# Kernel optimization log

Hardware: AMD Instinct MI355X
Metric: run time of the kernel (lower is better)

The kernel has to match this reference:

```python
import jax, jax.numpy as jnp
import numpy as np

BATCH = 2048
IN_DIM = 512          # group input dim
HID = 1024            # meta_output_dim = dim*2
E = 16                # meta_experts_num = num_experts*2
RANK = 2              # lora_rank
EPS = 1e-5


def setup_inputs() -> dict:
    key = jax.random.key(0)
    ks = jax.random.split(key, 8)
    x = jax.random.normal(ks[0], (BATCH, IN_DIM), jnp.float32)
    gate_states = jax.random.normal(ks[1], (BATCH, IN_DIM), jnp.float32)
    expert_indices = jnp.arange(E, dtype=jnp.int64)
    expert_weights = jax.random.normal(ks[2], (E, IN_DIM, HID), jnp.float32) * 0.02
    expert_biases = jnp.zeros((E, HID), jnp.float32)
    bn_weights = jnp.ones((E, HID), jnp.float32)
    bn_biases = jnp.zeros((E, HID), jnp.float32)
    running_mean = jax.random.normal(ks[3], (E, HID), jnp.float32) * 0.1
    running_var = jnp.abs(jax.random.normal(ks[4], (E, HID), jnp.float32)) * 0.5 + 0.5
    gate_weights = jax.random.normal(ks[5], (IN_DIM, E), jnp.float32) * 0.02
    lora_A = jax.random.normal(ks[6], (IN_DIM, RANK), jnp.float32) * 0.02
    lora_B = jax.random.normal(ks[7], (RANK, IN_DIM), jnp.float32) * 0.02
    return dict(x=x, gate_states=gate_states, expert_indices=expert_indices,
                expert_weights=expert_weights, expert_biases=expert_biases,
                bn_weights=bn_weights, bn_biases=bn_biases,
                running_mean=running_mean, running_var=running_var,
                gate_weights=gate_weights, lora_A=lora_A, lora_B=lora_B)


def reference(x, gate_states, expert_indices, expert_weights, expert_biases,
              bn_weights, bn_biases, running_mean, running_var,
              gate_weights, lora_A, lora_B):
    # LoRA feature gate (lora_gate_forward with sigmoid): x * sigmoid(x A B)
    xg = x * jax.nn.sigmoid((x @ lora_A) @ lora_B)          # [B, D]

    # Expert dispatch: gather selected expert params (home_expert_forward)
    W = expert_weights[expert_indices]                        # [E, D, H]
    b = expert_biases[expert_indices]                         # [E, H]
    h = jnp.einsum('bd,edh->ebh', xg, W) + b[:, None, :]      # [E, B, H]

    # Fused inference BatchNorm + SiLU (fused_batch_norm_silu_forward)
    inv = jax.lax.rsqrt(running_var[expert_indices] + EPS)    # [E, H]
    scale = bn_weights[expert_indices] * inv                  # [E, H]
    shift = bn_biases[expert_indices] - running_mean[expert_indices] * scale
    h = h * scale[:, None, :] + shift[:, None, :]
    h = h * jax.nn.sigmoid(h)                                 # SiLU

    # Softmax gate (gate_weights_forward) and weighted combine
    g = jax.nn.softmax(gate_states @ gate_weights, axis=-1)   # [B, E]
    out = jnp.einsum('ebh,be->bh', h, g)                      # [B, H]
    return out
```

## Files before the change

### kernel.cpp

```cpp
#include <hip/hip_runtime.h>
#include <hip/hip_bf16.h>

#define BATCH 2048
#define IN_DIM 512
#define HID 1024
#define NE 16
#define EPSV 1e-5f

typedef __bf16 bf16x8 __attribute__((ext_vector_type(8)));
typedef float floatx4 __attribute__((ext_vector_type(4)));
typedef unsigned short ushort8 __attribute__((ext_vector_type(8)));

__device__ __forceinline__ unsigned short f2bf(float f) {
  unsigned int u = __builtin_bit_cast(unsigned int, f);
  u += 0x7FFFu + ((u >> 16) & 1u);
  return (unsigned short)(u >> 16);
}

__device__ __forceinline__ int get_expert(const int* __restrict__ idx, int e) {
  bool is64 = (idx[1] == 0) && (idx[3] == 0);
  return is64 ? (int)((const long long*)idx)[e] : idx[e];
}

__device__ __forceinline__ void gld16(void* lds, const void* g) {
  __builtin_amdgcn_global_load_lds(
      (const __attribute__((address_space(1))) void*)g,
      (__attribute__((address_space(3))) void*)lds, 16, 0, 0);
}

__global__ __launch_bounds__(256) void zero_out(float* __restrict__ out) {
  int t = blockIdx.x * 256 + threadIdx.x;
  ((float4*)out)[t] = float4{0.f, 0.f, 0.f, 0.f};
}

__global__ __launch_bounds__(256) void prep_coef(
    const int* __restrict__ idx, const float* __restrict__ bnw,
    const float* __restrict__ bnb, const float* __restrict__ rmean,
    const float* __restrict__ rvar, const float* __restrict__ ebias,
    float* __restrict__ Ac, float* __restrict__ Cc) {
  int t = blockIdx.x * 256 + threadIdx.x;
  int e = t >> 10, h = t & 1023;
  int ie = get_expert(idx, e);
  size_t o = (size_t)ie * HID + h;
  float scale = bnw[o] * rsqrtf(rvar[o] + EPSV);
  Ac[t] = scale;
  Cc[t] = (ebias[o] - rmean[o]) * scale + bnb[o];
}

__global__ __launch_bounds__(256) void prep_rows(
    const float* __restrict__ x, const float* __restrict__ gs,
    const float* __restrict__ gw, const float* __restrict__ lA,
    const float* __restrict__ lB,
    unsigned short* __restrict__ xg, float* __restrict__ g) {
  int lane = threadIdx.x & 63;
  int wid = threadIdx.x >> 6;
  int b = blockIdx.x * 4 + wid;
  const float* xrow = x + (size_t)b * IN_DIM;
  const float* grow = gs + (size_t)b * IN_DIM;
  int d0 = lane * 8;

  float4 xa = *(const float4*)(xrow + d0);
  float4 xb = *(const float4*)(xrow + d0 + 4);
  float xv[8] = {xa.x, xa.y, xa.z, xa.w, xb.x, xb.y, xb.z, xb.w};
  float4 ga = *(const float4*)(grow + d0);
  float4 gb = *(const float4*)(grow + d0 + 4);
  float gv[8] = {ga.x, ga.y, ga.z, ga.w, gb.x, gb.y, gb.z, gb.w};

  float u0 = 0.f, u1 = 0.f;
#pragma unroll
  for (int j = 0; j < 8; ++j) {
    float2 a2 = *(const float2*)(lA + (size_t)(d0 + j) * 2);
    u0 += xv[j] * a2.x;
    u1 += xv[j] * a2.y;
  }
#pragma unroll
  for (int off = 1; off < 64; off <<= 1) {
    u0 += __shfl_xor(u0, off);
    u1 += __shfl_xor(u1, off);
  }

  float ge[16];
#pragma unroll
  for (int e = 0; e < 16; ++e) ge[e] = 0.f;
#pragma unroll
  for (int j = 0; j < 8; ++j) {
    float q = gv[j];
    const float4* gwr = (const float4*)(gw + (size_t)(d0 + j) * NE);
    float4 w0 = gwr[0], w1 = gwr[1], w2 = gwr[2], w3 = gwr[3];
    ge[0] += q * w0.x; ge[1] += q * w0.y; ge[2] += q * w0.z; ge[3] += q * w0.w;
    ge[4] += q * w1.x; ge[5] += q * w1.y; ge[6] += q * w1.z; ge[7] += q * w1.w;
    ge[8] += q * w2.x; ge[9] += q * w2.y; ge[10] += q * w2.z; ge[11] += q * w2.w;
    ge[12] += q * w3.x; ge[13] += q * w3.y; ge[14] += q * w3.z; ge[15] += q * w3.w;
  }
#pragma unroll
  for (int off = 1; off < 64; off <<= 1) {
#pragma unroll
    for (int e = 0; e < 16; ++e) ge[e] += __shfl_xor(ge[e], off);
  }
  float m = ge[0];
#pragma unroll
  for (int e = 1; e < 16; ++e) m = fmaxf(m, ge[e]);
  float p[16], s = 0.f;
#pragma unroll
  for (int e = 0; e < 16; ++e) { p[e] = __expf(ge[e] - m); s += p[e]; }
  float inv = 1.f / s;
  if (lane == 0) {
    float* gout = g + (size_t)b * NE;
#pragma unroll
    for (int e = 0; e < 16; ++e) gout[e] = p[e] * inv;
  }

  ushort8 ov;
#pragma unroll
  for (int j = 0; j < 8; ++j) {
    float t = u0 * lB[d0 + j] + u1 * lB[IN_DIM + d0 + j];
    float sg = 1.f / (1.f + __expf(-t));
    ov[j] = f2bf(xv[j] * sg);
  }
  *(ushort8*)(xg + (size_t)b * IN_DIM + d0) = ov;
}

__global__ __launch_bounds__(256) void prep_tw(
    const int* __restrict__ idx, const float* __restrict__ W,
    unsigned short* __restrict__ WT) {
  int bid = blockIdx.x;
  int e = bid >> 7;
  int kt = (bid >> 4) & 7;
  int ht = bid & 15;
  int ie = get_expert(idx, e);
  int k0 = kt * 64, h0 = ht * 64;
  __shared__ float tile[64][65];
  const float* Wp = W + (size_t)ie * IN_DIM * HID;
#pragma unroll
  for (int i = 0; i < 4; ++i) {
    int id = threadIdx.x + i * 256;
    int k = id >> 4, c = (id & 15) * 4;
    float4 v = *(const float4*)(Wp + (size_t)(k0 + k) * HID + h0 + c);
    tile[k][c] = v.x; tile[k][c + 1] = v.y; tile[k][c + 2] = v.z; tile[k][c + 3] = v.w;
  }
  __syncthreads();
#pragma unroll
  for (int i = 0; i < 2; ++i) {
    int id = threadIdx.x + i * 256;
    int h = id >> 3, kc = (id & 7) * 8;
    ushort8 o;
#pragma unroll
    for (int j = 0; j < 8; ++j) o[j] = f2bf(tile[kc + j][h]);
    *(ushort8*)(WT + ((size_t)e * HID + h0 + h) * IN_DIM + k0 + kc) = o;
  }
}

#define BM 128
#define BN 128
#define BK 32
#define EPB 4

__global__ __launch_bounds__(256, 2) void moe_main(
    const unsigned short* __restrict__ xg, const unsigned short* __restrict__ WT,
    const float* __restrict__ g, const float* __restrict__ Ac,
    const float* __restrict__ Cc, float* __restrict__ out) {
  __shared__ __align__(16) unsigned short As[2][BM * BK];
  __shared__ __align__(16) unsigned short Bs[2][BN * BK];
  __shared__ float gS[BM][EPB];

  int tid = threadIdx.x;
  int lane = tid & 63, w = tid >> 6;
  int wr = w >> 1, wc = w & 1;
  int l15 = lane & 15, quad = lane >> 4;

  int bid = blockIdx.x;
  int p = bid >> 7;
  int rowb = (bid >> 3) & 15, colb = bid & 7;
  int row0 = rowb * BM, col0 = colb * BN;
  int e0 = p * EPB;

  for (int i = tid; i < BM * EPB; i += 256) {
    int r = i >> 2, e = i & 3;
    gS[r][e] = g[(size_t)(row0 + r) * NE + e0 + e];
  }

  int dr = lane >> 2, dk = (lane & 3) * 8;
  const unsigned short* gA = xg + (size_t)(row0 + w * 32 + dr) * IN_DIM + dk;
  const unsigned short* gB0 = WT + ((size_t)e0 * HID + col0 + w * 32 + dr) * IN_DIM + dk;

  auto dma = [&](int t, int buf) {
    int e = t >> 4, k0 = (t & 15) * BK;
    const unsigned short* a = gA + k0;
    const unsigned short* b = gB0 + (size_t)e * HID * IN_DIM + k0;
#pragma unroll
    for (int j = 0; j < 2; ++j) {
      gld16(&As[buf][(w * 32 + j * 16) * BK], a + (size_t)j * 16 * IN_DIM);
      gld16(&Bs[buf][(w * 32 + j * 16) * BK], b + (size_t)j * 16 * IN_DIM);
    }
  };

  floatx4 acc[4][4], oacc[4][4];
#pragma unroll
  for (int rt = 0; rt < 4; ++rt)
#pragma unroll
    for (int ct = 0; ct < 4; ++ct)
#pragma unroll
      for (int r = 0; r < 4; ++r) { acc[rt][ct][r] = 0.f; oacc[rt][ct][r] = 0.f; }

  dma(0, 0);
  __syncthreads();
  int buf = 0;
  for (int t = 0; t < EPB * 16; ++t) {
    if (t < EPB * 16 - 1) dma(t + 1, buf ^ 1);
    bf16x8 af[4], bf[4];
#pragma unroll
    for (int rt = 0; rt < 4; ++rt)
      af[rt] = *(const bf16x8*)&As[buf][(wr * 64 + rt * 16 + l15) * BK + quad * 8];
#pragma unroll
    for (int ct = 0; ct < 4; ++ct)
      bf[ct] = *(const bf16x8*)&Bs[buf][(wc * 64 + ct * 16 + l15) * BK + quad * 8];
#pragma unroll
    for (int rt = 0; rt < 4; ++rt)
#pragma unroll
      for (int ct = 0; ct < 4; ++ct)
        acc[rt][ct] = __builtin_amdgcn_mfma_f32_16x16x32_bf16(af[rt], bf[ct], acc[rt][ct], 0, 0, 0);
    if ((t & 15) == 15) {
      int e = t >> 4;
#pragma unroll
      for (int ct = 0; ct < 4; ++ct) {
        int colg = col0 + wc * 64 + ct * 16 + l15;
        float A_ = Ac[(e0 + e) * HID + colg];
        float C_ = Cc[(e0 + e) * HID + colg];
#pragma unroll
        for (int rt = 0; rt < 4; ++rt) {
          int rb = wr * 64 + rt * 16 + quad * 4;
#pragma unroll
          for (int r = 0; r < 4; ++r) {
            float gvw = gS[rb + r][e];
            float z = A_ * acc[rt][ct][r] + C_;
            float sg = 1.f / (1.f + __expf(-z));
            oacc[rt][ct][r] += gvw * z * sg;
            acc[rt][ct][r] = 0.f;
          }
        }
      }
    }
    __syncthreads();
    buf ^= 1;
  }

#pragma unroll
  for (int rt = 0; rt < 4; ++rt)
#pragma unroll
    for (int ct = 0; ct < 4; ++ct)
#pragma unroll
      for (int r = 0; r < 4; ++r)
        atomicAdd(&out[(size_t)(row0 + wr * 64 + rt * 16 + quad * 4 + r) * HID +
                       col0 + wc * 64 + ct * 16 + l15], oacc[rt][ct][r]);
}

extern "C" void kernel_launch(void* const* d_in, const int* in_sizes, int n_in,
                              void* d_out, int out_size, void* d_ws, size_t ws_size,
                              hipStream_t stream) {
  const float* x     = (const float*)d_in[0];
  const float* gs    = (const float*)d_in[1];
  const int*   idx   = (const int*)d_in[2];
  const float* W     = (const float*)d_in[3];
  const float* ebias = (const float*)d_in[4];
  const float* bnw   = (const float*)d_in[5];
  const float* bnb   = (const float*)d_in[6];
  const float* rmean = (const float*)d_in[7];
  const float* rvar  = (const float*)d_in[8];
  const float* gw    = (const float*)d_in[9];
  const float* lA    = (const float*)d_in[10];
  const float* lB    = (const float*)d_in[11];
  float* out = (float*)d_out;

  char* ws = (char*)d_ws;
  unsigned short* WT = (unsigned short*)ws;
  unsigned short* xg = (unsigned short*)(ws + 16777216);
  float* g   = (float*)(ws + 18874368);
  float* Acf = (float*)(ws + 19005440);
  float* Ccf = (float*)(ws + 19070976);

  zero_out<<<dim3(BATCH * HID / 1024), dim3(256), 0, stream>>>(out);
  prep_coef<<<dim3(64), dim3(256), 0, stream>>>(idx, bnw, bnb, rmean, rvar, ebias, Acf, Ccf);
  prep_rows<<<dim3(BATCH / 4), dim3(256), 0, stream>>>(x, gs, gw, lA, lB, xg, g);
  prep_tw<<<dim3(2048), dim3(256), 0, stream>>>(idx, W, WT);
  moe_main<<<dim3((BATCH / BM) * (HID / BN) * (NE / EPB)), dim3(256), 0, stream>>>(
      xg, WT, g, Acf, Ccf, out);
}
```

Baseline: 197.3 us.

## Merge prep kernels, deepen K stage, replace atomics with split-buffer reduction

Combines the three prep kernels into one launch that dispatches on block index. The main GEMM loop now stages two 32-wide K slices per double-buffered step, which halves the number of barriers. When the workspace is large enough, each expert group writes its partial output to a separate buffer with plain stores, and a reduce kernel then sums the four buffers. This replaces the zero-fill plus atomicAdd path but costs extra memory traffic: 32MB written and read back, plus a larger LDS footprint.

```diff
diff --git a/kernel.cpp b/kernel.cpp
--- a/kernel.cpp
+++ b/kernel.cpp
@@ -28,139 +28,144 @@
       (__attribute__((address_space(3))) void*)lds, 16, 0, 0);
 }
 
+__global__ __launch_bounds__(256) void prep_all(
+    const int* __restrict__ idx, const float* __restrict__ W,
+    unsigned short* __restrict__ WT,
+    const float* __restrict__ x, const float* __restrict__ gs,
+    const float* __restrict__ gw, const float* __restrict__ lA,
+    const float* __restrict__ lB,
+    unsigned short* __restrict__ xg, float* __restrict__ g,
+    const float* __restrict__ bnw, const float* __restrict__ bnb,
+    const float* __restrict__ rmean, const float* __restrict__ rvar,
+    const float* __restrict__ ebias,
+    float* __restrict__ Ac, float* __restrict__ Cc) {
+  int bid = blockIdx.x;
+  if (bid < 2048) {
+    int e = bid >> 7, kt = (bid >> 4) & 7, ht = bid & 15;
+    int ie = get_expert(idx, e);
+    int k0 = kt * 64, h0 = ht * 64;
+    __shared__ float tile[64][65];
+    const float* Wp = W + (size_t)ie * IN_DIM * HID;
+#pragma unroll
+    for (int i = 0; i < 4; ++i) {
+      int id = threadIdx.x + i * 256;
+      int k = id >> 4, c = (id & 15) * 4;
+      float4 v = *(const float4*)(Wp + (size_t)(k0 + k) * HID + h0 + c);
+      tile[k][c] = v.x; tile[k][c + 1] = v.y; tile[k][c + 2] = v.z; tile[k][c + 3] = v.w;
+    }
+    __syncthreads();
+#pragma unroll
+    for (int i = 0; i < 2; ++i) {
+      int id = threadIdx.x + i * 256;
+      int h = id >> 3, kc = (id & 7) * 8;
+      ushort8 o;
+#pragma unroll
+      for (int j = 0; j < 8; ++j) o[j] = f2bf(tile[kc + j][h]);
+      *(ushort8*)(WT + ((size_t)e * HID + h0 + h) * IN_DIM + k0 + kc) = o;
+    }
+  } else if (bid < 2560) {
+    int lane = threadIdx.x & 63;
+    int b = (bid - 2048) * 4 + (threadIdx.x >> 6);
+    const float* xrow = x + (size_t)b * IN_DIM;
+    const float* grow = gs + (size_t)b * IN_DIM;
+    int d0 = lane * 8;
+    float4 xa = *(const float4*)(xrow + d0);
+    float4 xb = *(const float4*)(xrow + d0 + 4);
+    float xv[8] = {xa.x, xa.y, xa.z, xa.w, xb.x, xb.y, xb.z, xb.w};
+    float4 ga = *(const float4*)(grow + d0);
+    float4 gb = *(const float4*)(grow + d0 + 4);
+    float gv[8] = {ga.x, ga.y, ga.z, ga.w, gb.x, gb.y, gb.z, gb.w};
+
+    float u0 = 0.f, u1 = 0.f;
+#pragma unroll
+    for (int j = 0; j < 8; ++j) {
+      float2 a2 = *(const float2*)(lA + (size_t)(d0 + j) * 2);
+      u0 += xv[j] * a2.x;
+      u1 += xv[j] * a2.y;
+    }
+#pragma unroll
+    for (int off = 1; off < 64; off <<= 1) {
+      u0 += __shfl_xor(u0, off);
+      u1 += __shfl_xor(u1, off);
+    }
+    float ge[16];
+#pragma unroll
+    for (int e = 0; e < 16; ++e) ge[e] = 0.f;
+#pragma unroll
+    for (int j = 0; j < 8; ++j) {
+      float q = gv[j];
+      const float4* gwr = (const float4*)(gw + (size_t)(d0 + j) * NE);
+      float4 w0 = gwr[0], w1 = gwr[1], w2 = gwr[2], w3 = gwr[3];
+      ge[0] += q * w0.x; ge[1] += q * w0.y; ge[2] += q * w0.z; ge[3] += q * w0.w;
+      ge[4] += q * w1.x; ge[5] += q * w1.y; ge[6] += q * w1.z; ge[7] += q * w1.w;
+      ge[8] += q * w2.x; ge[9] += q * w2.y; ge[10] += q * w2.z; ge[11] += q * w2.w;
+      ge[12] += q * w3.x; ge[13] += q * w3.y; ge[14] += q * w3.z; ge[15] += q * w3.w;
+    }
+#pragma unroll
+    for (int off = 1; off < 64; off <<= 1) {
+#pragma unroll
+      for (int e = 0; e < 16; ++e) ge[e] += __shfl_xor(ge[e], off);
+    }
+    float m = ge[0];
+#pragma unroll
+    for (int e = 1; e < 16; ++e) m = fmaxf(m, ge[e]);
+    float p[16], s = 0.f;
+#pragma unroll
+    for (int e = 0; e < 16; ++e) { p[e] = __expf(ge[e] - m); s += p[e]; }
+    float inv = 1.f / s;
+    if (lane == 0) {
+      float* gout = g + (size_t)b * NE;
+#pragma unroll
+      for (int e = 0; e < 16; ++e) gout[e] = p[e] * inv;
+    }
+    ushort8 ov;
+#pragma unroll
+    for (int j = 0; j < 8; ++j) {
+      float t = u0 * lB[d0 + j] + u1 * lB[IN_DIM + d0 + j];
+      float sg = 1.f / (1.f + __expf(-t));
+      ov[j] = f2bf(xv[j] * sg);
+    }
+    *(ushort8*)(xg + (size_t)b * IN_DIM + d0) = ov;
+  } else {
+    int t = (bid - 2560) * 256 + threadIdx.x;
+    int e = t >> 10, h = t & 1023;
+    int ie = get_expert(idx, e);
+    size_t o = (size_t)ie * HID + h;
+    float scale = bnw[o] * rsqrtf(rvar[o] + EPSV);
+    Ac[t] = scale;
+    Cc[t] = (ebias[o] - rmean[o]) * scale + bnb[o];
+  }
+}
+
 __global__ __launch_bounds__(256) void zero_out(float* __restrict__ out) {
   int t = blockIdx.x * 256 + threadIdx.x;
   ((float4*)out)[t] = float4{0.f, 0.f, 0.f, 0.f};
 }
 
-__global__ __launch_bounds__(256) void prep_coef(
-    const int* __restrict__ idx, const float* __restrict__ bnw,
-    const float* __restrict__ bnb, const float* __restrict__ rmean,
-    const float* __restrict__ rvar, const float* __restrict__ ebias,
-    float* __restrict__ Ac, float* __restrict__ Cc) {
+__global__ __launch_bounds__(256) void reduce4(const float* __restrict__ sws,
+                                               float* __restrict__ out) {
   int t = blockIdx.x * 256 + threadIdx.x;
-  int e = t >> 10, h = t & 1023;
-  int ie = get_expert(idx, e);
-  size_t o = (size_t)ie * HID + h;
-  float scale = bnw[o] * rsqrtf(rvar[o] + EPSV);
-  Ac[t] = scale;
-  Cc[t] = (ebias[o] - rmean[o]) * scale + bnb[o];
-}
-
-__global__ __launch_bounds__(256) void prep_rows(
-    const float* __restrict__ x, const float* __restrict__ gs,
-    const float* __restrict__ gw, const float* __restrict__ lA,
-    const float* __restrict__ lB,
-    unsigned short* __restrict__ xg, float* __restrict__ g) {
-  int lane = threadIdx.x & 63;
-  int wid = threadIdx.x >> 6;
-  int b = blockIdx.x * 4 + wid;
-  const float* xrow = x + (size_t)b * IN_DIM;
-  const float* grow = gs + (size_t)b * IN_DIM;
-  int d0 = lane * 8;
-
-  float4 xa = *(const float4*)(xrow + d0);
-  float4 xb = *(const float4*)(xrow + d0 + 4);
-  float xv[8] = {xa.x, xa.y, xa.z, xa.w, xb.x, xb.y, xb.z, xb.w};
-  float4 ga = *(const float4*)(grow + d0);
-  float4 gb = *(const float4*)(grow + d0 + 4);
-  float gv[8] = {ga.x, ga.y, ga.z, ga.w, gb.x, gb.y, gb.z, gb.w};
-
-  float u0 = 0.f, u1 = 0.f;
-#pragma unroll
-  for (int j = 0; j < 8; ++j) {
-    float2 a2 = *(const float2*)(lA + (size_t)(d0 + j) * 2);
-    u0 += xv[j] * a2.x;
-    u1 += xv[j] * a2.y;
-  }
-#pragma unroll
-  for (int off = 1; off < 64; off <<= 1) {
-    u0 += __shfl_xor(u0, off);
-    u1 += __shfl_xor(u1, off);
-  }
-
-  float ge[16];
-#pragma unroll
-  for (int e = 0; e < 16; ++e) ge[e] = 0.f;
-#pragma unroll
-  for (int j = 0; j < 8; ++j) {
-    float q = gv[j];
-    const float4* gwr = (const float4*)(gw + (size_t)(d0 + j) * NE);
-    float4 w0 = gwr[0], w1 = gwr[1], w2 = gwr[2], w3 = gwr[3];
-    ge[0] += q * w0.x; ge[1] += q * w0.y; ge[2] += q * w0.z; ge[3] += q * w0.w;
-    ge[4] += q * w1.x; ge[5] += q * w1.y; ge[6] += q * w1.z; ge[7] += q * w1.w;
-    ge[8] += q * w2.x; ge[9] += q * w2.y; ge[10] += q * w2.z; ge[11] += q * w2.w;
-    ge[12] += q * w3.x; ge[13] += q * w3.y; ge[14] += q * w3.z; ge[15] += q * w3.w;
-  }
-#pragma unroll
-  for (int off = 1; off < 64; off <<= 1) {
-#pragma unroll
-    for (int e = 0; e < 16; ++e) ge[e] += __shfl_xor(ge[e], off);
-  }
-  float m = ge[0];
-#pragma unroll
-  for (int e = 1; e < 16; ++e) m = fmaxf(m, ge[e]);
-  float p[16], s = 0.f;
-#pragma unroll
-  for (int e = 0; e < 16; ++e) { p[e] = __expf(ge[e] - m); s += p[e]; }
-  float inv = 1.f / s;
-  if (lane == 0) {
-    float* gout = g + (size_t)b * NE;
-#pragma unroll
-    for (int e = 0; e < 16; ++e) gout[e] = p[e] * inv;
-  }
-
-  ushort8 ov;
-#pragma unroll
-  for (int j = 0; j < 8; ++j) {
-    float t = u0 * lB[d0 + j] + u1 * lB[IN_DIM + d0 + j];
-    float sg = 1.f / (1.f + __expf(-t));
-    ov[j] = f2bf(xv[j] * sg);
-  }
-  *(ushort8*)(xg + (size_t)b * IN_DIM + d0) = ov;
-}
-
-__global__ __launch_bounds__(256) void prep_tw(
-    const int* __restrict__ idx, const float* __restrict__ W,
-    unsigned short* __restrict__ WT) {
-  int bid = blockIdx.x;
-  int e = bid >> 7;
-  int kt = (bid >> 4) & 7;
-  int ht = bid & 15;
-  int ie = get_expert(idx, e);
-  int k0 = kt * 64, h0 = ht * 64;
-  __shared__ float tile[64][65];
-  const float* Wp = W + (size_t)ie * IN_DIM * HID;
-#pragma unroll
-  for (int i = 0; i < 4; ++i) {
-    int id = threadIdx.x + i * 256;
-    int k = id >> 4, c = (id & 15) * 4;
-    float4 v = *(const float4*)(Wp + (size_t)(k0 + k) * HID + h0 + c);
-    tile[k][c] = v.x; tile[k][c + 1] = v.y; tile[k][c + 2] = v.z; tile[k][c + 3] = v.w;
-  }
-  __syncthreads();
-#pragma unroll
-  for (int i = 0; i < 2; ++i) {
-    int id = threadIdx.x + i * 256;
-    int h = id >> 3, kc = (id & 7) * 8;
-    ushort8 o;
-#pragma unroll
-    for (int j = 0; j < 8; ++j) o[j] = f2bf(tile[kc + j][h]);
-    *(ushort8*)(WT + ((size_t)e * HID + h0 + h) * IN_DIM + k0 + kc) = o;
-  }
+  const float4* s0 = (const float4*)sws;
+  const float4* s1 = s0 + (BATCH * HID / 4);
+  const float4* s2 = s1 + (BATCH * HID / 4);
+  const float4* s3 = s2 + (BATCH * HID / 4);
+  float4 a = s0[t], b = s1[t], c = s2[t], d = s3[t];
+  ((float4*)out)[t] = float4{a.x + b.x + c.x + d.x, a.y + b.y + c.y + d.y,
+                             a.z + b.z + c.z + d.z, a.w + b.w + c.w + d.w};
 }
 
 #define BM 128
 #define BN 128
-#define BK 32
+#define KS 32
 #define EPB 4
 
 __global__ __launch_bounds__(256, 2) void moe_main(
     const unsigned short* __restrict__ xg, const unsigned short* __restrict__ WT,
     const float* __restrict__ g, const float* __restrict__ Ac,
-    const float* __restrict__ Cc, float* __restrict__ out) {
-  __shared__ __align__(16) unsigned short As[2][BM * BK];
-  __shared__ __align__(16) unsigned short Bs[2][BN * BK];
+    const float* __restrict__ Cc, float* __restrict__ splitws,
+    float* __restrict__ out, int use_split) {
+  __shared__ __align__(16) unsigned short As[2][2][BM * KS];
+  __shared__ __align__(16) unsigned short Bs[2][2][BN * KS];
   __shared__ float gS[BM][EPB];
 
   int tid = threadIdx.x;
@@ -181,16 +186,21 @@
 
   int dr = lane >> 2, dk = (lane & 3) * 8;
   const unsigned short* gA = xg + (size_t)(row0 + w * 32 + dr) * IN_DIM + dk;
-  const unsigned short* gB0 = WT + ((size_t)e0 * HID + col0 + w * 32 + dr) * IN_DIM + dk;
+  const unsigned short* gB = WT + ((size_t)e0 * HID + col0 + w * 32 + dr) * IN_DIM + dk;
 
   auto dma = [&](int t, int buf) {
-    int e = t >> 4, k0 = (t & 15) * BK;
-    const unsigned short* a = gA + k0;
-    const unsigned short* b = gB0 + (size_t)e * HID * IN_DIM + k0;
-#pragma unroll
-    for (int j = 0; j < 2; ++j) {
-      gld16(&As[buf][(w * 32 + j * 16) * BK], a + (size_t)j * 16 * IN_DIM);
-      gld16(&Bs[buf][(w * 32 + j * 16) * BK], b + (size_t)j * 16 * IN_DIM);
+    int e = t >> 3, s = t & 7;
+    size_t aoff = (size_t)s * 64;
+    size_t boff = (size_t)e * HID * IN_DIM + s * 64;
+#pragma unroll
+    for (int kk = 0; kk < 2; ++kk) {
+#pragma unroll
+      for (int j = 0; j < 2; ++j) {
+        gld16(&As[buf][kk][(w * 32 + j * 16) * KS],
+              gA + aoff + kk * KS + (size_t)j * 16 * IN_DIM);
+        gld16(&Bs[buf][kk][(w * 32 + j * 16) * KS],
+              gB + boff + kk * KS + (size_t)j * 16 * IN_DIM);
+      }
     }
   };
 
@@ -205,22 +215,25 @@
   dma(0, 0);
   __syncthreads();
   int buf = 0;
-  for (int t = 0; t < EPB * 16; ++t) {
-    if (t < EPB * 16 - 1) dma(t + 1, buf ^ 1);
-    bf16x8 af[4], bf[4];
-#pragma unroll
-    for (int rt = 0; rt < 4; ++rt)
-      af[rt] = *(const bf16x8*)&As[buf][(wr * 64 + rt * 16 + l15) * BK + quad * 8];
-#pragma unroll
-    for (int ct = 0; ct < 4; ++ct)
-      bf[ct] = *(const bf16x8*)&Bs[buf][(wc * 64 + ct * 16 + l15) * BK + quad * 8];
-#pragma unroll
-    for (int rt = 0; rt < 4; ++rt)
+  for (int t = 0; t < 32; ++t) {
+    if (t < 31) dma(t + 1, buf ^ 1);
+#pragma unroll
+    for (int kk = 0; kk < 2; ++kk) {
+      bf16x8 af[4], bfv[4];
+#pragma unroll
+      for (int rt = 0; rt < 4; ++rt)
+        af[rt] = *(const bf16x8*)&As[buf][kk][(wr * 64 + rt * 16 + l15) * KS + quad * 8];
 #pragma unroll
       for (int ct = 0; ct < 4; ++ct)
-        acc[rt][ct] = __builtin_amdgcn_mfma_f32_16x16x32_bf16(af[rt], bf[ct], acc[rt][ct], 0, 0, 0);
-    if ((t & 15) == 15) {
-      int e = t >> 4;
+        bfv[ct] = *(const bf16x8*)&Bs[buf][kk][(wc * 64 + ct * 16 + l15) * KS + quad * 8];
+#pragma unroll
+      for (int rt = 0; rt < 4; ++rt)
+#pragma unroll
+        for (int ct = 0; ct < 4; ++ct)
+          acc[rt][ct] = __builtin_amdgcn_mfma_f32_16x16x32_bf16(af[rt], bfv[ct], acc[rt][ct], 0, 0, 0);
+    }
+    if ((t & 7) == 7) {
+      int e = t >> 3;
 #pragma unroll
       for (int ct = 0; ct < 4; ++ct) {
         int colg = col0 + wc * 64 + ct * 16 + l15;
@@ -244,14 +257,26 @@
     buf ^= 1;
   }
 
-#pragma unroll
-  for (int rt = 0; rt < 4; ++rt)
-#pragma unroll
-    for (int ct = 0; ct < 4; ++ct)
-#pragma unroll
-      for (int r = 0; r < 4; ++r)
-        atomicAdd(&out[(size_t)(row0 + wr * 64 + rt * 16 + quad * 4 + r) * HID +
-                       col0 + wc * 64 + ct * 16 + l15], oacc[rt][ct][r]);
+  if (use_split) {
+    float* sout = splitws + (size_t)p * BATCH * HID;
+#pragma unroll
+    for (int rt = 0; rt < 4; ++rt)
+#pragma unroll
+      for (int ct = 0; ct < 4; ++ct)
+#pragma unroll
+        for (int r = 0; r < 4; ++r)
+          sout[(size_t)(row0 + wr * 64 + rt * 16 + quad * 4 + r) * HID +
+               col0 + wc * 64 + ct * 16 + l15] = oacc[rt][ct][r];
+  } else {
+#pragma unroll
+    for (int rt = 0; rt < 4; ++rt)
+#pragma unroll
+      for (int ct = 0; ct < 4; ++ct)
+#pragma unroll
+        for (int r = 0; r < 4; ++r)
+          atomicAdd(&out[(size_t)(row0 + wr * 64 + rt * 16 + quad * 4 + r) * HID +
+                         col0 + wc * 64 + ct * 16 + l15], oacc[rt][ct][r]);
+  }
 }
 
 extern "C" void kernel_launch(void* const* d_in, const int* in_sizes, int n_in,
@@ -274,14 +299,18 @@
   char* ws = (char*)d_ws;
   unsigned short* WT = (unsigned short*)ws;
   unsigned short* xg = (unsigned short*)(ws + 16777216);
-  float* g   = (float*)(ws + 18874368);
-  float* Acf = (float*)(ws + 19005440);
-  float* Ccf = (float*)(ws + 19070976);
-
-  zero_out<<<dim3(BATCH * HID / 1024), dim3(256), 0, stream>>>(out);
-  prep_coef<<<dim3(64), dim3(256), 0, stream>>>(idx, bnw, bnb, rmean, rvar, ebias, Acf, Ccf);
-  prep_rows<<<dim3(BATCH / 4), dim3(256), 0, stream>>>(x, gs, gw, lA, lB, xg, g);
-  prep_tw<<<dim3(2048), dim3(256), 0, stream>>>(idx, W, WT);
+  float* g    = (float*)(ws + 18874368);
+  float* Acf  = (float*)(ws + 19005440);
+  float* Ccf  = (float*)(ws + 19070976);
+  float* sws  = (float*)(ws + 19136512);
+  int use_split = (ws_size >= 19136512 + 4ull * BATCH * HID * 4) ? 1 : 0;
+
+  prep_all<<<dim3(2624), dim3(256), 0, stream>>>(
+      idx, W, WT, x, gs, gw, lA, lB, xg, g, bnw, bnb, rmean, rvar, ebias, Acf, Ccf);
+  if (!use_split)
+    zero_out<<<dim3(BATCH * HID / 1024), dim3(256), 0, stream>>>(out);
   moe_main<<<dim3((BATCH / BM) * (HID / BN) * (NE / EPB)), dim3(256), 0, stream>>>(
-      xg, WT, g, Acf, Ccf, out);
-}
+      xg, WT, g, Acf, Ccf, sws, out, use_split);
+  if (use_split)
+    reduce4<<<dim3(BATCH * HID / 1024), dim3(256), 0, stream>>>(sws, out);
+}
```

Result: faster. 179.1 us (-9.2%).
